# Kernel tuning notes

Hardware: AMD Instinct MI355X
Metric: run time of the kernel (lower is better)

Reference implementation:

```python
import jax, jax.numpy as jnp
import numpy as np

N, G, E, H, OUT, MAX_N = 131072, 256, 384, 6, 256, 1024
DH = E // H  # 64


def _make_sizes():
    # variable-length segments summing exactly to N, each in [1, MAX_N]
    rng = np.random.default_rng(0)
    raw = rng.integers(128, 896, G).astype(np.int64)
    diff = int(N - raw.sum())
    q, r = divmod(diff, G)
    sizes = raw + q
    sizes[:r] += 1
    assert sizes.sum() == N and sizes.min() >= 1 and sizes.max() <= MAX_N
    return sizes


def setup_inputs() -> dict:
    key = jax.random.key(0)
    ks = jax.random.split(key, 8)
    s = 1.0 / np.sqrt(E)
    return {
        "node_feat": jax.random.normal(ks[0], (N, E), jnp.float32),
        "sizes": jnp.asarray(_make_sizes(), jnp.int32),
        "query": jax.random.normal(ks[1], (E,), jnp.float32),
        "Wq": jax.random.normal(ks[2], (E, E), jnp.float32) * s,
        "bq": jnp.zeros((E,), jnp.float32),
        "Wk": jax.random.normal(ks[3], (E, E), jnp.float32) * s,
        "bk": jnp.zeros((E,), jnp.float32),
        "Wv": jax.random.normal(ks[4], (E, E), jnp.float32) * s,
        "bv": jnp.zeros((E,), jnp.float32),
        "Wo": jax.random.normal(ks[5], (E, E), jnp.float32) * s,
        "bo": jnp.zeros((E,), jnp.float32),
        "Wp": jax.random.normal(ks[6], (OUT, E), jnp.float32) * s,
        "bp": jnp.zeros((OUT,), jnp.float32),
    }


def reference(node_feat, sizes, query, Wq, bq, Wk, bk, Wv, bv, Wo, bo, Wp, bp):
    # segment offsets and padded gather indices
    offsets = jnp.cumsum(sizes) - sizes                      # [G]
    pos = jnp.arange(MAX_N)
    idx = jnp.clip(offsets[:, None] + pos[None, :], 0, N - 1)  # [G, MAX_N]
    mask = pos[None, :] < sizes[:, None]                     # [G, MAX_N]

    # project K/V on the flat node table (one big GEMM), then gather into padded form
    k_flat = node_feat @ Wk.T + bk                           # [N, E]
    v_flat = node_feat @ Wv.T + bv
    k = k_flat[idx].reshape(G, MAX_N, H, DH)
    v = v_flat[idx].reshape(G, MAX_N, H, DH)

    # single shared query token, pre-scaled (PyTorch MHA scales q by 1/sqrt(head_dim))
    q = ((query @ Wq.T + bq) * (1.0 / np.sqrt(DH))).reshape(H, DH)

    scores = jnp.einsum('hd,gnhd->ghn', q, k)                # [G, H, MAX_N]
    scores = jnp.where(mask[:, None, :], scores, -1e30)
    attn = jax.nn.softmax(scores, axis=-1)
    pooled = jnp.einsum('ghn,gnhd->ghd', attn, v).reshape(G, E)

    out = pooled @ Wo.T + bo                                 # MHA out_proj
    return out @ Wp.T + bp                                   # final proj  [G, OUT]
```

## Files before the change

### kernel.cpp

```cpp
#include <hip/hip_runtime.h>
#include <math.h>

#define NN 131072
#define G  256
#define E  384
#define H  6
#define DH 64
#define OUTD 256
#define MAXN 1024

#define CHK 32
#define SLOTS 32
#define PART_STRIDE 2316

#define WS_QK   0
#define WS_C    2304
#define WS_OFF  2432
#define WS_QV   2944
#define WS_WL   3328
#define WS_M    11520
#define WS_CS   11776
#define WS_PART 12288
#define WS_WVT  (WS_PART + G*SLOTS*PART_STRIDE)
#define WS_WOT  (WS_WVT + E*E)
#define WS_WPT  (WS_WOT + E*E)

__global__ __launch_bounds__(256) void k0a_scan_qv(
    const int* __restrict__ sizes, const float* __restrict__ query,
    const float* __restrict__ Wq, const float* __restrict__ bq,
    float* __restrict__ wsf) {
  const int tid = threadIdx.x;
  if (blockIdx.x == 0) {
    __shared__ int s_scan[G];
    __shared__ int s_scan2[G];
    const int sz = sizes[tid];
    s_scan[tid] = sz;
    const int nch = (sz + CHK - 1) >> 5;
    s_scan2[tid] = nch;
    __syncthreads();
    for (int d = 1; d < G; d <<= 1) {
      int t = (tid >= d) ? s_scan[tid - d] : 0;
      int t2 = (tid >= d) ? s_scan2[tid - d] : 0;
      __syncthreads();
      s_scan[tid] += t;
      s_scan2[tid] += t2;
      __syncthreads();
    }
    ((int*)(wsf + WS_OFF))[tid] = s_scan[tid] - sz;
    const int pos = s_scan2[tid] - nch;
    ((int*)(wsf + WS_CS))[tid] = pos;
    int* wl = (int*)(wsf + WS_WL);
    for (int s = 0; s < nch; s++) wl[pos + s] = (tid << 5) | s;
    if (tid == G - 1) ((int*)(wsf + WS_M))[0] = s_scan2[G - 1];
  } else {
    const int lane = tid & 63;
    const int i = (blockIdx.x - 1) * 4 + (tid >> 6);
    float a = 0.f;
#pragma unroll
    for (int j = 0; j < 6; j++)
      a += Wq[(size_t)i * E + j * 64 + lane] * query[j * 64 + lane];
#pragma unroll
    for (int mm = 1; mm < 64; mm <<= 1) a += __shfl_xor(a, mm, 64);
    if (lane == 0) wsf[WS_QV + i] = 0.125f * (a + bq[i]);
  }
}

__global__ __launch_bounds__(256) void k0b_qk(
    const float* __restrict__ Wk, const float* __restrict__ bk,
    float* __restrict__ wsf) {
  __shared__ float qv_s[64];
  __shared__ float ps[256];
  const int h = blockIdx.x / 6, ec = blockIdx.x % 6;
  const int tid = threadIdx.x;
  if (tid < 64) qv_s[tid] = wsf[WS_QV + h * 64 + tid];
  __syncthreads();
  const int el = tid & 63, dq = tid >> 6;
  float a = 0.f;
#pragma unroll 4
  for (int d = dq * 16; d < dq * 16 + 16; d++)
    a += qv_s[d] * Wk[(size_t)(h * 64 + d) * E + ec * 64 + el];
  ps[tid] = a;
  __syncthreads();
  if (tid < 64)
    wsf[WS_QK + h * E + ec * 64 + tid] =
        ps[tid] + ps[64 + tid] + ps[128 + tid] + ps[192 + tid];
  if (ec == 0 && tid < 64) {
    float p = qv_s[tid] * bk[h * 64 + tid];
#pragma unroll
    for (int mm = 1; mm < 64; mm <<= 1) p += __shfl_xor(p, mm, 64);
    if (tid == 0) wsf[WS_C + h] = p;
  }
}

__global__ __launch_bounds__(256) void k0t_transpose(
    const float* __restrict__ Wv, const float* __restrict__ Wo,
    const float* __restrict__ Wp, float* __restrict__ wsf) {
  __shared__ float s[64][65];
  const int b = blockIdx.x;
  const float* src;
  float* dst;
  int R, tr, tc;
  if (b < 36)      { src = Wv; dst = wsf + WS_WVT; R = 384; tr = b / 6;        tc = b % 6; }
  else if (b < 72) { src = Wo; dst = wsf + WS_WOT; R = 384; tr = (b - 36) / 6; tc = (b - 36) % 6; }
  else             { src = Wp; dst = wsf + WS_WPT; R = 256; tr = (b - 72) / 6; tc = (b - 72) % 6; }
  const int r0 = tr * 64, c0 = tc * 64;
#pragma unroll
  for (int k = 0; k < 16; k++) {
    int idx = k * 256 + threadIdx.x;
    int r = idx >> 6, cc = idx & 63;
    s[r][cc] = src[(size_t)(r0 + r) * E + c0 + cc];
  }
  __syncthreads();
#pragma unroll
  for (int k = 0; k < 16; k++) {
    int idx = k * 256 + threadIdx.x;
    int cc = idx >> 6, r = idx & 63;
    dst[(size_t)(c0 + cc) * R + r0 + r] = s[r][cc];
  }
}

template <int CTRL>
__device__ __forceinline__ float dpp_radd(float v) {
  int t = __builtin_amdgcn_update_dpp(0, __float_as_int(v), CTRL, 0xf, 0xf, true);
  return v + __int_as_float(t);
}
__device__ __forceinline__ float wave_sum64(float v) {
  v = dpp_radd<0xB1>(v);
  v = dpp_radd<0x4E>(v);
  v = dpp_radd<0x141>(v);
  v = dpp_radd<0x140>(v);
  v += __shfl_xor(v, 16, 64);
  v += __shfl_xor(v, 32, 64);
  return v;
}

__global__ __launch_bounds__(64, 2) void k12_fused(
    const float* __restrict__ x, const int* __restrict__ sizes,
    float* __restrict__ wsf) {
  const int M = ((const int*)(wsf + WS_M))[0];
  const int it = blockIdx.x;
  if (it >= M) return;
  const int lane = threadIdx.x;
  const int item = ((const int*)(wsf + WS_WL))[it];
  const int g = item >> 5, s = item & 31;
  const int rem = sizes[g] - s * CHK;
  const int clen = rem < CHK ? rem : CHK;
  const int n0 = ((const int*)(wsf + WS_OFF))[g] + s * CHK;

  float qk[6][6];
#pragma unroll
  for (int h = 0; h < 6; h++)
#pragma unroll
    for (int k = 0; k < 6; k++) qk[h][k] = wsf[WS_QK + h * E + k * 64 + lane];

  float m[6], l[6], acc[6][6];
#pragma unroll
  for (int h = 0; h < 6; h++) {
    m[h] = -3.0e38f;
    l[h] = 0.f;
#pragma unroll
    for (int k = 0; k < 6; k++) acc[h][k] = 0.f;
  }

  const float* xp = x + (size_t)n0 * E + lane;

  float x0[6], x1[6], x2[6];
#define LOADX(buf, idx)                                            \
  {                                                                \
    const float* p_ = xp + (size_t)(idx) * E;                      \
    _Pragma("unroll") for (int k_ = 0; k_ < 6; k_++)               \
        buf[k_] = p_[k_ * 64];                                     \
  }
  LOADX(x0, 0);
  {
    const int i1 = (1 < clen) ? 1 : (clen - 1);
    LOADX(x1, i1);
  }

  for (int n = 0; n < clen; n++) {
    {
      const int i2 = (n + 2 < clen) ? (n + 2) : (clen - 1);
      LOADX(x2, i2);
    }
    float sr[6];
#pragma unroll
    for (int h = 0; h < 6; h++) {
      float a = qk[h][0] * x0[0];
#pragma unroll
      for (int k = 1; k < 6; k++) a = fmaf(qk[h][k], x0[k], a);
      sr[h] = a;
    }
#pragma unroll
    for (int h = 0; h < 6; h++) sr[h] = wave_sum64(sr[h]);
    bool upd = false;
#pragma unroll
    for (int h = 0; h < 6; h++) upd = upd || (sr[h] > m[h] + 8.0f);
    if (upd) {
#pragma unroll
      for (int h = 0; h < 6; h++) {
        const float nm = fmaxf(m[h], sr[h]);
        const float f = __expf(m[h] - nm);
        m[h] = nm;
        l[h] *= f;
#pragma unroll
        for (int k = 0; k < 6; k++) acc[h][k] *= f;
      }
    }
#pragma unroll
    for (int h = 0; h < 6; h++) {
      const float p = __expf(sr[h] - m[h]);
      l[h] += p;
#pragma unroll
      for (int k = 0; k < 6; k++) acc[h][k] = fmaf(p, x0[k], acc[h][k]);
    }
#pragma unroll
    for (int k = 0; k < 6; k++) {
      x0[k] = x1[k];
      x1[k] = x2[k];
    }
  }
#undef LOADX

  float* pslot = wsf + WS_PART + (size_t)it * PART_STRIDE;
#pragma unroll
  for (int h = 0; h < 6; h++)
#pragma unroll
    for (int k = 0; k < 6; k++)
      pslot[h * E + k * 64 + lane] = acc[h][k];
  if (lane < 6) {
    float vm = m[0], vl = l[0];
#pragma unroll
    for (int h = 1; h < 6; h++) {
      vm = (lane == h) ? m[h] : vm;
      vl = (lane == h) ? l[h] : vl;
    }
    pslot[2304 + lane] = vm;
    pslot[2310 + lane] = vl;
  }
}

__global__ __launch_bounds__(768) void k3_group(
    const float* __restrict__ wsf, const int* __restrict__ sizes,
    const float* __restrict__ bv, const float* __restrict__ bo,
    const float* __restrict__ bp, float* __restrict__ out) {
  __shared__ float xb[H * E];
  __shared__ float pooled[E];
  __shared__ float om[E];
  __shared__ float ps[768];
  __shared__ float msh[SLOTS][H], lsh[SLOTS][H], wgt[SLOTS][H];
  __shared__ float linv[H];
  const int tid = threadIdx.x;
  const int g = blockIdx.x;
  const int nch = (sizes[g] + CHK - 1) >> 5;
  const int base_s = ((const int*)(wsf + WS_CS))[g];
  const float* pg = wsf + WS_PART + (size_t)base_s * PART_STRIDE;
  const float* wvt = wsf + WS_WVT;
  const float* wot = wsf + WS_WOT;
  const float* wpt = wsf + WS_WPT;

  if (tid < SLOTS * H) {
    const int s2 = tid / H, h2 = tid % H;
    if (s2 < nch) {
      msh[s2][h2] = pg[(size_t)s2 * PART_STRIDE + 2304 + h2];
      lsh[s2][h2] = pg[(size_t)s2 * PART_STRIDE + 2310 + h2];
    }
  }
  __syncthreads();
  if (tid < H) {
    float m = -3.0e38f;
    for (int s = 0; s < nch; s++) m = fmaxf(m, msh[s][tid]);
    float L = 0.f;
    for (int s = 0; s < nch; s++) {
      float wv_ = __expf(msh[s][tid] - m);
      wgt[s][tid] = wv_;
      L += lsh[s][tid] * wv_;
    }
    linv[tid] = 1.f / L;
  }
  __syncthreads();
  for (int idx = tid; idx < H * E; idx += 768) {
    const int h = idx / E;
    const float* pp = pg + idx;
    float a0 = 0.f, a1 = 0.f, a2 = 0.f, a3 = 0.f;
    int s2 = 0;
    for (; s2 + 3 < nch; s2 += 4) {
      a0 += pp[(size_t)(s2 + 0) * PART_STRIDE] * wgt[s2 + 0][h];
      a1 += pp[(size_t)(s2 + 1) * PART_STRIDE] * wgt[s2 + 1][h];
      a2 += pp[(size_t)(s2 + 2) * PART_STRIDE] * wgt[s2 + 2][h];
      a3 += pp[(size_t)(s2 + 3) * PART_STRIDE] * wgt[s2 + 3][h];
    }
    for (; s2 < nch; s2++) a0 += pp[(size_t)s2 * PART_STRIDE] * wgt[s2][h];
    xb[idx] = ((a0 + a1) + (a2 + a3)) * linv[h];
  }
  __syncthreads();

  {
    const int i = tid % 384, ks = tid / 384;
    const float* xh = xb + (i >> 6) * E + ks * 192;
    const float* wp_ = wvt + (size_t)(ks * 192) * E + i;
    float a0 = 0.f, a1 = 0.f, a2 = 0.f, a3 = 0.f;
#pragma unroll 4
    for (int e = 0; e < 192; e += 4) {
      a0 += wp_[(size_t)(e + 0) * E] * xh[e + 0];
      a1 += wp_[(size_t)(e + 1) * E] * xh[e + 1];
      a2 += wp_[(size_t)(e + 2) * E] * xh[e + 2];
      a3 += wp_[(size_t)(e + 3) * E] * xh[e + 3];
    }
    ps[tid] = (a0 + a1) + (a2 + a3);
  }
  __syncthreads();
  if (tid < 384) pooled[tid] = ps[tid] + ps[384 + tid] + bv[tid];
  __syncthreads();

  {
    const int i = tid % 384, ks = tid / 384;
    const float* xh = pooled + ks * 192;
    const float* wp_ = wot + (size_t)(ks * 192) * E + i;
    float a0 = 0.f, a1 = 0.f, a2 = 0.f, a3 = 0.f;
#pragma unroll 4
    for (int e = 0; e < 192; e += 4) {
      a0 += wp_[(size_t)(e + 0) * E] * xh[e + 0];
      a1 += wp_[(size_t)(e + 1) * E] * xh[e + 1];
      a2 += wp_[(size_t)(e + 2) * E] * xh[e + 2];
      a3 += wp_[(size_t)(e + 3) * E] * xh[e + 3];
    }
    ps[tid] = (a0 + a1) + (a2 + a3);
  }
  __syncthreads();
  if (tid < 384) om[tid] = ps[tid] + ps[384 + tid] + bo[tid];
  __syncthreads();

  {
    const int o = tid % 256, ks = tid / 256;
    const float* xh = om + ks * 128;
    const float* wp_ = wpt + (size_t)(ks * 128) * OUTD + o;
    float a0 = 0.f, a1 = 0.f, a2 = 0.f, a3 = 0.f;
#pragma unroll 4
    for (int e = 0; e < 128; e += 4) {
      a0 += wp_[(size_t)(e + 0) * OUTD] * xh[e + 0];
      a1 += wp_[(size_t)(e + 1) * OUTD] * xh[e + 1];
      a2 += wp_[(size_t)(e + 2) * OUTD] * xh[e + 2];
      a3 += wp_[(size_t)(e + 3) * OUTD] * xh[e + 3];
    }
    ps[tid] = (a0 + a1) + (a2 + a3);
  }
  __syncthreads();
  if (tid < 256)
    out[(size_t)g * OUTD + tid] = ps[tid] + ps[256 + tid] + ps[512 + tid] + bp[tid];
}

extern "C" void kernel_launch(void* const* d_in, const int* in_sizes, int n_in,
                              void* d_out, int out_size, void* d_ws, size_t ws_size,
                              hipStream_t stream) {
  const float* x     = (const float*)d_in[0];
  const int*   sizes = (const int*)d_in[1];
  const float* query = (const float*)d_in[2];
  const float* Wq    = (const float*)d_in[3];
  const float* bq    = (const float*)d_in[4];
  const float* Wk    = (const float*)d_in[5];
  const float* bk    = (const float*)d_in[6];
  const float* Wv    = (const float*)d_in[7];
  const float* bv    = (const float*)d_in[8];
  const float* Wo    = (const float*)d_in[9];
  const float* bo    = (const float*)d_in[10];
  const float* Wp    = (const float*)d_in[11];
  const float* bp    = (const float*)d_in[12];
  float* wsf = (float*)d_ws;
  float* out = (float*)d_out;

  hipLaunchKernelGGL(k0a_scan_qv, dim3(97), dim3(256), 0, stream,
                     sizes, query, Wq, bq, wsf);
  hipLaunchKernelGGL(k0b_qk, dim3(36), dim3(256), 0, stream, Wk, bk, wsf);
  hipLaunchKernelGGL(k0t_transpose, dim3(96), dim3(256), 0, stream,
                     Wv, Wo, Wp, wsf);
  hipLaunchKernelGGL(k12_fused, dim3(4352), dim3(64), 0, stream,
                     x, sizes, wsf);
  hipLaunchKernelGGL(k3_group, dim3(G), dim3(768), 0, stream,
                     wsf, sizes, bv, bo, bp, out);
}
```

Measured before the change: 351.4 us.

## Fuse chunked attention pooling and group projection into one per-group kernel

Replaces the per-chunk worklist kernel and the separate group-merge kernel with one kernel that runs a 768-thread block per segment. Each block's 12 waves stride over the segment's rows and keep online-softmax state in registers, then merge the 12 partial states through shared memory before doing the V/O/P projections in the same block. This drops the worklist build, the large global partial-state buffer and its write/read round trip, and one kernel launch. The cost is only 256 blocks of parallelism and uneven per-block work because segment lengths vary, which may underuse the GPU compared with the finer chunk decomposition.

```diff
diff --git a/kernel.cpp b/kernel.cpp
--- a/kernel.cpp
+++ b/kernel.cpp
@@ -9,19 +9,11 @@
 #define OUTD 256
 #define MAXN 1024
 
-#define CHK 32
-#define SLOTS 32
-#define PART_STRIDE 2316
-
 #define WS_QK   0
 #define WS_C    2304
 #define WS_OFF  2432
 #define WS_QV   2944
-#define WS_WL   3328
-#define WS_M    11520
-#define WS_CS   11776
-#define WS_PART 12288
-#define WS_WVT  (WS_PART + G*SLOTS*PART_STRIDE)
+#define WS_WVT  12288
 #define WS_WOT  (WS_WVT + E*E)
 #define WS_WPT  (WS_WOT + E*E)
 
@@ -32,26 +24,16 @@
   const int tid = threadIdx.x;
   if (blockIdx.x == 0) {
     __shared__ int s_scan[G];
-    __shared__ int s_scan2[G];
     const int sz = sizes[tid];
     s_scan[tid] = sz;
-    const int nch = (sz + CHK - 1) >> 5;
-    s_scan2[tid] = nch;
     __syncthreads();
     for (int d = 1; d < G; d <<= 1) {
       int t = (tid >= d) ? s_scan[tid - d] : 0;
-      int t2 = (tid >= d) ? s_scan2[tid - d] : 0;
       __syncthreads();
       s_scan[tid] += t;
-      s_scan2[tid] += t2;
       __syncthreads();
     }
     ((int*)(wsf + WS_OFF))[tid] = s_scan[tid] - sz;
-    const int pos = s_scan2[tid] - nch;
-    ((int*)(wsf + WS_CS))[tid] = pos;
-    int* wl = (int*)(wsf + WS_WL);
-    for (int s = 0; s < nch; s++) wl[pos + s] = (tid << 5) | s;
-    if (tid == G - 1) ((int*)(wsf + WS_M))[0] = s_scan2[G - 1];
   } else {
     const int lane = tid & 63;
     const int i = (blockIdx.x - 1) * 4 + (tid >> 6);
@@ -84,12 +66,6 @@
   if (tid < 64)
     wsf[WS_QK + h * E + ec * 64 + tid] =
         ps[tid] + ps[64 + tid] + ps[128 + tid] + ps[192 + tid];
-  if (ec == 0 && tid < 64) {
-    float p = qv_s[tid] * bk[h * 64 + tid];
-#pragma unroll
-    for (int mm = 1; mm < 64; mm <<= 1) p += __shfl_xor(p, mm, 64);
-    if (tid == 0) wsf[WS_C + h] = p;
-  }
 }
 
 __global__ __launch_bounds__(256) void k0t_transpose(
@@ -134,18 +110,24 @@
   return v;
 }
 
-__global__ __launch_bounds__(64, 2) void k12_fused(
+__global__ __launch_bounds__(768, 3) void k12g_fused(
     const float* __restrict__ x, const int* __restrict__ sizes,
-    float* __restrict__ wsf) {
-  const int M = ((const int*)(wsf + WS_M))[0];
-  const int it = blockIdx.x;
-  if (it >= M) return;
-  const int lane = threadIdx.x;
-  const int item = ((const int*)(wsf + WS_WL))[it];
-  const int g = item >> 5, s = item & 31;
-  const int rem = sizes[g] - s * CHK;
-  const int clen = rem < CHK ? rem : CHK;
-  const int n0 = ((const int*)(wsf + WS_OFF))[g] + s * CHK;
+    const float* __restrict__ bv, const float* __restrict__ bo,
+    const float* __restrict__ bp, float* __restrict__ out,
+    const float* __restrict__ wsf) {
+  __shared__ float xsl[4][H * E];
+  __shared__ float ps[768];
+  __shared__ float pooled[E];
+  __shared__ float om[E];
+  __shared__ float msh[12][H], lsh[12][H], wgts[12][H];
+  __shared__ float linv[H];
+
+  const int tid = threadIdx.x;
+  const int lane = tid & 63;
+  const int w = tid >> 6;
+  const int g = blockIdx.x;
+  const int sz = sizes[g];
+  const int n0 = ((const int*)(wsf + WS_OFF))[g];
 
   float qk[6][6];
 #pragma unroll
@@ -162,137 +144,129 @@
     for (int k = 0; k < 6; k++) acc[h][k] = 0.f;
   }
 
-  const float* xp = x + (size_t)n0 * E + lane;
-
-  float x0[6], x1[6], x2[6];
-#define LOADX(buf, idx)                                            \
+  const float* xp = x + (size_t)(n0 + w) * E + lane;
+  const int cnt = (sz > w) ? ((sz - w + 11) / 12) : 0;
+
+  float x0[6], x1[6];
+#define LOADX(buf, i)                                              \
   {                                                                \
-    const float* p_ = xp + (size_t)(idx) * E;                      \
+    const float* p_ = xp + (size_t)(i) * (12 * E);                 \
     _Pragma("unroll") for (int k_ = 0; k_ < 6; k_++)               \
         buf[k_] = p_[k_ * 64];                                     \
   }
-  LOADX(x0, 0);
-  {
-    const int i1 = (1 < clen) ? 1 : (clen - 1);
-    LOADX(x1, i1);
-  }
-
-  for (int n = 0; n < clen; n++) {
-    {
-      const int i2 = (n + 2 < clen) ? (n + 2) : (clen - 1);
-      LOADX(x2, i2);
-    }
-    float sr[6];
+#define COMPUTE(xv)                                                          \
+  {                                                                          \
+    float sr[6];                                                             \
+    _Pragma("unroll") for (int h_ = 0; h_ < 6; h_++) {                       \
+      float a_ = qk[h_][0] * xv[0];                                          \
+      _Pragma("unroll") for (int k_ = 1; k_ < 6; k_++)                       \
+          a_ = fmaf(qk[h_][k_], xv[k_], a_);                                 \
+      sr[h_] = a_;                                                           \
+    }                                                                        \
+    _Pragma("unroll") for (int h_ = 0; h_ < 6; h_++)                         \
+        sr[h_] = wave_sum64(sr[h_]);                                         \
+    bool upd_ = false;                                                       \
+    _Pragma("unroll") for (int h_ = 0; h_ < 6; h_++)                         \
+        upd_ = upd_ || (sr[h_] > m[h_] + 8.0f);                              \
+    if (upd_) {                                                              \
+      _Pragma("unroll") for (int h_ = 0; h_ < 6; h_++) {                     \
+        const float nm_ = fmaxf(m[h_], sr[h_]);                              \
+        const float f_ = __expf(m[h_] - nm_);                                \
+        m[h_] = nm_;                                                         \
+        l[h_] *= f_;                                                         \
+        _Pragma("unroll") for (int k_ = 0; k_ < 6; k_++) acc[h_][k_] *= f_;  \
+      }                                                                      \
+    }                                                                        \
+    _Pragma("unroll") for (int h_ = 0; h_ < 6; h_++) {                       \
+      const float p_ = __expf(sr[h_] - m[h_]);                               \
+      l[h_] += p_;                                                           \
+      _Pragma("unroll") for (int k_ = 0; k_ < 6; k_++)                       \
+          acc[h_][k_] = fmaf(p_, xv[k_], acc[h_][k_]);                       \
+    }                                                                        \
+  }
+
+  if (cnt > 0) {
+    LOADX(x0, 0);
+    int i = 0;
+    while (true) {
+      int ip = (i + 1 < cnt) ? i + 1 : i;
+      LOADX(x1, ip);
+      COMPUTE(x0);
+      if (++i >= cnt) break;
+      ip = (i + 1 < cnt) ? i + 1 : i;
+      LOADX(x0, ip);
+      COMPUTE(x1);
+      if (++i >= cnt) break;
+    }
+  }
+#undef LOADX
+#undef COMPUTE
+
+  if (lane == 0) {
 #pragma unroll
     for (int h = 0; h < 6; h++) {
-      float a = qk[h][0] * x0[0];
-#pragma unroll
-      for (int k = 1; k < 6; k++) a = fmaf(qk[h][k], x0[k], a);
-      sr[h] = a;
-    }
-#pragma unroll
-    for (int h = 0; h < 6; h++) sr[h] = wave_sum64(sr[h]);
-    bool upd = false;
-#pragma unroll
-    for (int h = 0; h < 6; h++) upd = upd || (sr[h] > m[h] + 8.0f);
-    if (upd) {
-#pragma unroll
-      for (int h = 0; h < 6; h++) {
-        const float nm = fmaxf(m[h], sr[h]);
-        const float f = __expf(m[h] - nm);
-        m[h] = nm;
-        l[h] *= f;
-#pragma unroll
-        for (int k = 0; k < 6; k++) acc[h][k] *= f;
-      }
-    }
-#pragma unroll
-    for (int h = 0; h < 6; h++) {
-      const float p = __expf(sr[h] - m[h]);
-      l[h] += p;
-#pragma unroll
-      for (int k = 0; k < 6; k++) acc[h][k] = fmaf(p, x0[k], acc[h][k]);
-    }
-#pragma unroll
-    for (int k = 0; k < 6; k++) {
-      x0[k] = x1[k];
-      x1[k] = x2[k];
-    }
-  }
-#undef LOADX
-
-  float* pslot = wsf + WS_PART + (size_t)it * PART_STRIDE;
-#pragma unroll
-  for (int h = 0; h < 6; h++)
-#pragma unroll
-    for (int k = 0; k < 6; k++)
-      pslot[h * E + k * 64 + lane] = acc[h][k];
-  if (lane < 6) {
-    float vm = m[0], vl = l[0];
-#pragma unroll
-    for (int h = 1; h < 6; h++) {
-      vm = (lane == h) ? m[h] : vm;
-      vl = (lane == h) ? l[h] : vl;
-    }
-    pslot[2304 + lane] = vm;
-    pslot[2310 + lane] = vl;
-  }
-}
-
-__global__ __launch_bounds__(768) void k3_group(
-    const float* __restrict__ wsf, const int* __restrict__ sizes,
-    const float* __restrict__ bv, const float* __restrict__ bo,
-    const float* __restrict__ bp, float* __restrict__ out) {
-  __shared__ float xb[H * E];
-  __shared__ float pooled[E];
-  __shared__ float om[E];
-  __shared__ float ps[768];
-  __shared__ float msh[SLOTS][H], lsh[SLOTS][H], wgt[SLOTS][H];
-  __shared__ float linv[H];
-  const int tid = threadIdx.x;
-  const int g = blockIdx.x;
-  const int nch = (sizes[g] + CHK - 1) >> 5;
-  const int base_s = ((const int*)(wsf + WS_CS))[g];
-  const float* pg = wsf + WS_PART + (size_t)base_s * PART_STRIDE;
+      msh[w][h] = m[h];
+      lsh[w][h] = l[h];
+    }
+  }
+  __syncthreads();
+  if (tid < 6) {
+    const int h = tid;
+    float M = -3.0e38f;
+    for (int s = 0; s < 12; s++) M = fmaxf(M, msh[s][h]);
+    float L = 0.f;
+    for (int s = 0; s < 12; s++) {
+      const float wv_ = __expf(msh[s][h] - M);
+      wgts[s][h] = wv_;
+      L += lsh[s][h] * wv_;
+    }
+    linv[h] = 1.0f / L;
+  }
+  __syncthreads();
+  {
+    float wg[6];
+#pragma unroll
+    for (int h = 0; h < 6; h++) wg[h] = wgts[w][h];
+#pragma unroll
+    for (int h = 0; h < 6; h++)
+#pragma unroll
+      for (int k = 0; k < 6; k++) acc[h][k] *= wg[h];
+  }
+  {
+    float* xs = &xsl[w & 3][0];
+    if (w < 4) {
+#pragma unroll
+      for (int h = 0; h < 6; h++)
+#pragma unroll
+        for (int k = 0; k < 6; k++) xs[h * E + k * 64 + lane] = acc[h][k];
+    }
+    __syncthreads();
+    if (w >= 4 && w < 8) {
+#pragma unroll
+      for (int h = 0; h < 6; h++)
+#pragma unroll
+        for (int k = 0; k < 6; k++) xs[h * E + k * 64 + lane] += acc[h][k];
+    }
+    __syncthreads();
+    if (w >= 8) {
+#pragma unroll
+      for (int h = 0; h < 6; h++)
+#pragma unroll
+        for (int k = 0; k < 6; k++) xs[h * E + k * 64 + lane] += acc[h][k];
+    }
+    __syncthreads();
+  }
+  for (int idx = tid; idx < H * E; idx += 768) {
+    const int h = idx / E;
+    xsl[0][idx] = ((xsl[0][idx] + xsl[1][idx]) + (xsl[2][idx] + xsl[3][idx]))
+                  * linv[h];
+  }
+  __syncthreads();
+
+  const float* xb = &xsl[0][0];
   const float* wvt = wsf + WS_WVT;
   const float* wot = wsf + WS_WOT;
   const float* wpt = wsf + WS_WPT;
-
-  if (tid < SLOTS * H) {
-    const int s2 = tid / H, h2 = tid % H;
-    if (s2 < nch) {
-      msh[s2][h2] = pg[(size_t)s2 * PART_STRIDE + 2304 + h2];
-      lsh[s2][h2] = pg[(size_t)s2 * PART_STRIDE + 2310 + h2];
-    }
-  }
-  __syncthreads();
-  if (tid < H) {
-    float m = -3.0e38f;
-    for (int s = 0; s < nch; s++) m = fmaxf(m, msh[s][tid]);
-    float L = 0.f;
-    for (int s = 0; s < nch; s++) {
-      float wv_ = __expf(msh[s][tid] - m);
-      wgt[s][tid] = wv_;
-      L += lsh[s][tid] * wv_;
-    }
-    linv[tid] = 1.f / L;
-  }
-  __syncthreads();
-  for (int idx = tid; idx < H * E; idx += 768) {
-    const int h = idx / E;
-    const float* pp = pg + idx;
-    float a0 = 0.f, a1 = 0.f, a2 = 0.f, a3 = 0.f;
-    int s2 = 0;
-    for (; s2 + 3 < nch; s2 += 4) {
-      a0 += pp[(size_t)(s2 + 0) * PART_STRIDE] * wgt[s2 + 0][h];
-      a1 += pp[(size_t)(s2 + 1) * PART_STRIDE] * wgt[s2 + 1][h];
-      a2 += pp[(size_t)(s2 + 2) * PART_STRIDE] * wgt[s2 + 2][h];
-      a3 += pp[(size_t)(s2 + 3) * PART_STRIDE] * wgt[s2 + 3][h];
-    }
-    for (; s2 < nch; s2++) a0 += pp[(size_t)s2 * PART_STRIDE] * wgt[s2][h];
-    xb[idx] = ((a0 + a1) + (a2 + a3)) * linv[h];
-  }
-  __syncthreads();
 
   {
     const int i = tid % 384, ks = tid / 384;
@@ -373,8 +347,6 @@
   hipLaunchKernelGGL(k0b_qk, dim3(36), dim3(256), 0, stream, Wk, bk, wsf);
   hipLaunchKernelGGL(k0t_transpose, dim3(96), dim3(256), 0, stream,
                      Wv, Wo, Wp, wsf);
-  hipLaunchKernelGGL(k12_fused, dim3(4352), dim3(64), 0, stream,
-                     x, sizes, wsf);
-  hipLaunchKernelGGL(k3_group, dim3(G), dim3(768), 0, stream,
-                     wsf, sizes, bv, bo, bp, out);
-}
+  hipLaunchKernelGGL(k12g_fused, dim3(G), dim3(768), 0, stream,
+                     x, sizes, bv, bo, bp, out, wsf);
+}
```

Result: faster. 338.9 us (-3.6%).
